# Kernel tuning notes

Hardware: AMD Instinct MI355X
Metric: run time of the kernel (lower is better)

Reference implementation:

```python
import jax, jax.numpy as jnp
import numpy as np

BIT = 128
Y_P = 0.5
RIGHT = BIT / 8.0
LEFT = RIGHT / 2.0
UB = BIT / 2.0
ALPHA = 0.1
PCT_NUM, PCT_DEN = 9, 10  # percent = 9/10
C_COEF = (1.0 / RIGHT) * np.log(Y_P / (99.0 * (1.0 - Y_P)))  # slope c (constant since y_p fixed)
A_COEF = -1.0 / (LEFT * C_COEF) * np.log(99.0 * Y_P / (1.0 - Y_P))  # hard-branch factor a
# with y_p=0.5: d = -c*BP, g = -a*c*BP, so f_easy = c*(x-BP), f_hard = a*c*(x-BP)


def setup_inputs() -> dict:
    key = jax.random.key(0)
    k1, k2 = jax.random.split(key)
    N, C = 6144, 200
    u = jax.random.normal(k1, (N, BIT), dtype=jnp.float32)
    labels = jax.random.randint(k2, (N,), 0, C)
    y = jax.nn.one_hot(labels, C, dtype=jnp.int32)
    ind = jnp.arange(N, dtype=jnp.int32)  # unused dataset indices
    return {"u": u, "y": y, "ind": ind}


def reference(u, y, ind):
    sg = jax.lax.stop_gradient
    N = u.shape[0]
    uh = jnp.tanh(u)
    s = (y @ y.T) > 0                      # [N,N] bool similarity (diagonal is True)
    inner = uh @ uh.T                      # [N,N]
    n_sim = s.sum(axis=1)                  # int per-row similar count
    n_dis = N - n_sim
    fn_sim = n_sim.astype(jnp.float32)
    fn_dis = n_dis.astype(jnp.float32)
    idx = jnp.arange(N)[None, :]

    meanS = jnp.clip(jnp.where(s, inner, 0.0).sum(1) / jnp.maximum(fn_sim, 1.0), 0.0, UB)
    meanDS = jnp.clip(jnp.where(s, 0.0, inner).sum(1) / jnp.maximum(fn_dis, 1.0), 0.0, UB)

    dis_sorted = jnp.sort(jnp.where(s, -jnp.inf, inner), axis=1)
    start_dis = (n_dis * PCT_NUM) // PCT_DEN          # int(len*0.9)
    tail_mask = idx >= (N - n_dis + start_dis)[:, None]
    tail_cnt = jnp.maximum((n_dis - start_dis).astype(jnp.float32), 1.0)
    dMax = jnp.clip(jnp.where(tail_mask, dis_sorted, 0.0).sum(1) / tail_cnt, 0.0, UB)

    sim_sorted = jnp.sort(jnp.where(s, inner, jnp.inf), axis=1)
    start_sim = (n_sim * PCT_NUM) // PCT_DEN
    head_mask = idx < (n_sim - start_sim)[:, None]
    head_cnt = jnp.maximum((n_sim - start_sim).astype(jnp.float32), 1.0)
    sMin = jnp.clip(jnp.where(head_mask, sim_sorted, 0.0).sum(1) / head_cnt, 0.0, UB)

    # .item() in the original detaches these -> stop_gradient
    meanS, meanDS, dMax, sMin = map(sg, (meanS, meanDS, dMax, sMin))
    BP = meanS - (UB - meanS) / UB * jnp.abs(meanS - dMax)      # [N]
    BPd = meanDS + meanDS / UB * jnp.abs(meanDS - sMin)         # [N]

    # similar-pair loss: f + log(1+exp(-f)) == softplus(f)
    dc = inner - BP[:, None]
    f_sim = jnp.where(inner > BP[:, None], C_COEF * dc, A_COEF * C_COEF * dc)
    mask_sim = s & (inner != BP[:, None])             # == BP excluded in torch indexing
    cnt_sim = jnp.maximum(mask_sim.sum(1).astype(jnp.float32), 1.0)
    row_pos = jnp.where(mask_sim, jax.nn.softplus(f_sim), 0.0).sum(1) / cnt_sim

    # dissimilar-pair loss: log(1+exp(-f)) == softplus(-f)
    dcd = inner - BPd[:, None]
    f_dis = jnp.where(inner < BPd[:, None], C_COEF * dcd, A_COEF * C_COEF * dcd)
    mask_dis = (~s) & (inner != BPd[:, None])
    cnt_dis = jnp.maximum(mask_dis.sum(1).astype(jnp.float32), 1.0)
    row_neg = jnp.where(mask_dis, jax.nn.softplus(-f_dis), 0.0).sum(1) / cnt_dis

    valid = (n_sim > 0) & (n_dis > 0)
    count = valid.sum().astype(jnp.float32)
    posL = jnp.where(count > 0, jnp.where(valid, row_pos, 0.0).sum() / jnp.maximum(count, 1.0), 0.0)
    navL = jnp.where(count > 0, jnp.where(valid, row_neg, 0.0).sum() / jnp.maximum(count, 1.0), 0.0)

    q_loss = ALPHA * jnp.mean((uh - jnp.sign(uh)) ** 2)
    return posL + navL + q_loss
```

## Files before the change

kernel.cpp:

```cpp
#include <hip/hip_runtime.h>
#include <cstdint>

#define NROW 6144
#define KDIM 128
#define NLAB 200
#define C_COEF (-0.28719499063341177f)
#define UBV 64.0f

typedef _Float16 f16x8 __attribute__((ext_vector_type(8)));
typedef float f32x4 __attribute__((ext_vector_type(4)));
typedef __attribute__((address_space(1))) const void as1c_void;
typedef __attribute__((address_space(3))) void as3_void;

__device__ __forceinline__ float softplus_f(float x){
  return fmaxf(x, 0.f) + __logf(1.f + __expf(-fabsf(x)));
}
__device__ __forceinline__ float waveRedF(float v){
#pragma unroll
  for (int o = 32; o; o >>= 1) v += __shfl_down(v, o, 64);
  return v;
}
__device__ __forceinline__ float bfRedF(float v){
#pragma unroll
  for (int o = 32; o; o >>= 1) v += __shfl_xor(v, o, 64);
  return v;
}
__device__ __forceinline__ int bfRedI(int v){
#pragma unroll
  for (int o = 32; o; o >>= 1) v += __shfl_xor(v, o, 64);
  return v;
}
__device__ __forceinline__ int bfMaxI(int v){
#pragma unroll
  for (int o = 32; o; o >>= 1){ int x = __shfl_xor(v, o, 64); v = v > x ? v : x; }
  return v;
}
__device__ __forceinline__ float bfMaxF(float v){
#pragma unroll
  for (int o = 32; o; o >>= 1) v = fmaxf(v, __shfl_xor(v, o, 64));
  return v;
}
__device__ __forceinline__ int bucket_of(float v){
  int b = (int)floorf(v * 2.f) + 128;
  return b < 0 ? 0 : (b > 255 ? 255 : b);
}

__global__ void k_label(const int* __restrict__ y, unsigned char* __restrict__ lab,
                        int* __restrict__ cnt){
  const int row = blockIdx.x;
  const int t = threadIdx.x;
  if (t < NLAB){
    if (y[(size_t)row * NLAB + t] != 0){
      lab[row] = (unsigned char)t;
      atomicAdd(&cnt[t], 1);
    }
  }
}

__global__ __launch_bounds__(192) void k_clsmask(const unsigned char* __restrict__ lab,
                                                 unsigned* __restrict__ cm){
  const int c = blockIdx.x;
  const int w = threadIdx.x;
  const uint4* p = (const uint4*)(lab + w * 32);
  uint4 a = p[0], b = p[1];
  unsigned words[8] = {a.x, a.y, a.z, a.w, b.x, b.y, b.z, b.w};
  unsigned bits = 0;
#pragma unroll
  for (int j = 0; j < 8; j++)
#pragma unroll
    for (int i = 0; i < 4; i++)
      if (((words[j] >> (8 * i)) & 255u) == (unsigned)c) bits |= 1u << (4 * j + i);
  cm[c * 192 + w] = bits;
}

__global__ __launch_bounds__(256) void k_tanh(const float* __restrict__ u,
    _Float16* __restrict__ uhswz, float* __restrict__ accf){
  const int tid = threadIdx.x;
  const int gid = blockIdx.x * 256 + tid;
  const int row = gid >> 4;
  const int h = gid & 15;
  const int g = h ^ (row & 7);
  const float* sp = u + (size_t)row * KDIM + g * 8;
  float q = 0.f;
  f16x8 o;
#pragma unroll
  for (int t = 0; t < 8; t++){
    float x = sp[t];
    float e2 = __expf(2.f * x);
    float th = 1.f - 2.f * __builtin_amdgcn_rcpf(e2 + 1.f);
    float sg = (th > 0.f) ? 1.f : ((th < 0.f) ? -1.f : 0.f);
    float d = th - sg;
    q += d * d;
    o[t] = (_Float16)th;
  }
  *(f16x8*)(uhswz + (size_t)row * KDIM + h * 8) = o;
  q = waveRedF(q);
  __shared__ float qb[4];
  if ((tid & 63) == 0) qb[tid >> 6] = q;
  __syncthreads();
  if (tid == 0) atomicAdd(&accf[0], qb[0] + qb[1] + qb[2] + qb[3]);
}

__global__ __launch_bounds__(256) void k_mm(const _Float16* __restrict__ A,
    _Float16* __restrict__ out, int row0){
  __shared__ __align__(16) _Float16 SH[2 * 128 * KDIM];
  _Float16* As = SH;
  _Float16* Bs = SH + 128 * KDIM;
  const int tid = threadIdx.x;
  const int wav = tid >> 6, lane = tid & 63;
  const int bj = blockIdx.x, bi = blockIdx.y;

  const char* Ag = (const char*)(A + (size_t)(row0 + bi * 128) * KDIM);
  const char* Bg = (const char*)(A + (size_t)(bj * 128) * KDIM);
  char* Asb = (char*)As;
  char* Bsb = (char*)Bs;
#pragma unroll
  for (int t = 0; t < 8; t++){
    const int ub = wav * 8192 + t * 1024;
    __builtin_amdgcn_global_load_lds((as1c_void*)(Ag + ub + lane * 16),
                                     (as3_void*)(Asb + ub), 16, 0, 0);
    __builtin_amdgcn_global_load_lds((as1c_void*)(Bg + ub + lane * 16),
                                     (as3_void*)(Bsb + ub), 16, 0, 0);
  }
  __syncthreads();

  const int quad = lane >> 4, l16 = lane & 15;
  const int wm = (wav >> 1) * 64, wn = (wav & 1) * 64;
  f32x4 acc[4][4];
#pragma unroll
  for (int im = 0; im < 4; im++)
#pragma unroll
    for (int in = 0; in < 4; in++)
      acc[im][in] = (f32x4){0.f, 0.f, 0.f, 0.f};

#pragma unroll
  for (int kb = 0; kb < 4; kb++){
    f16x8 af[4], bf[4];
#pragma unroll
    for (int i = 0; i < 4; i++){
      const int m = wm + i * 16 + l16;
      const int gidx = kb * 4 + quad;
      af[i] = *(const f16x8*)(Asb + m * 256 + ((gidx ^ (m & 7)) << 4));
      const int n = wn + i * 16 + l16;
      bf[i] = *(const f16x8*)(Bsb + n * 256 + ((gidx ^ (n & 7)) << 4));
    }
#pragma unroll
    for (int im = 0; im < 4; im++)
#pragma unroll
      for (int in = 0; in < 4; in++)
        acc[im][in] = __builtin_amdgcn_mfma_f32_16x16x32_f16(af[im], bf[in], acc[im][in], 0, 0, 0);
  }
  __syncthreads();

  _Float16* Cs = SH;
#pragma unroll
  for (int im = 0; im < 4; im++)
#pragma unroll
    for (int in = 0; in < 4; in++)
#pragma unroll
      for (int r = 0; r < 4; r++){
        const int rl = wm + im * 16 + quad * 4 + r;
        const int cl = wn + in * 16 + l16;
        Cs[rl * 132 + cl] = (_Float16)acc[im][in][r];
      }
  __syncthreads();

  _Float16* obase = out + (size_t)(bi * 128) * NROW + (size_t)bj * 128;
  const int s = tid & 15;
#pragma unroll
  for (int i = 0; i < 8; i++){
    const int r = (tid >> 4) + i * 16;
    f16x8 vv = *(const f16x8*)(Cs + r * 132 + s * 8);
    *(f16x8*)(obase + (size_t)r * NROW + s * 8) = vv;
  }
}

__global__ __launch_bounds__(256) void k_stats(const _Float16* __restrict__ buf,
    const unsigned char* __restrict__ lab, const int* __restrict__ cnt,
    const unsigned* __restrict__ cm,
    float* __restrict__ rowRes, int row0){
  __shared__ int   histS[4][256];
  __shared__ float simvS[4][512];
  __shared__ float candS[4][512];
  const int tid = threadIdx.x;
  const int lane = tid & 63;
  const int wav = tid >> 6;
  const int lrow = blockIdx.x * 4 + wav;
  const int row = row0 + lrow;
  const int myl = lab[row];
  const int n_sim = cnt[myl];
  const int n_dis = NROW - n_sim;
  if (n_dis == 0 || n_sim == 0) return;
  const int k1 = n_dis - (n_dis * 9) / 10;
  const int k2 = n_sim - (n_sim * 9) / 10;

  int*   hist = histS[wav];
  float* simv = simvS[wav];
  float* cand = candS[wav];
  *(int4*)&hist[lane * 4] = make_int4(0, 0, 0, 0);

  const f16x8* src = (const f16x8*)(buf + (size_t)lrow * NROW);
  const unsigned char* mrow = (const unsigned char*)(cm + (size_t)myl * 192);
  const unsigned long long below = (1ull << lane) - 1ull;

  float sumS = 0.f, sumD = 0.f;
  int nsB = 0;
#pragma unroll 1
  for (int it = 0; it < 12; ++it){
    f16x8 h8 = src[it * 64 + lane];
    unsigned m8 = (unsigned)mrow[it * 64 + lane];
#pragma unroll
    for (int e = 0; e < 8; e++){
      float v = (float)h8[e];
      bool sim = (m8 >> e) & 1u;
      unsigned long long bm = __ballot(sim);
      int pos = nsB + __builtin_popcountll(bm & below);
      nsB += __builtin_popcountll(bm);
      if (sim){
        sumS += v;
        if (pos < 512) simv[pos] = v;
      } else {
        sumD += v;
        atomicAdd(&hist[bucket_of(v)], 1);
      }
    }
  }
  sumS = bfRedF(sumS);
  sumD = bfRedF(sumD);
  const int ns = nsB < 512 ? nsB : 512;

  int cArr[4];
  cArr[0] = hist[4 * lane];
  cArr[1] = hist[4 * lane + 1];
  cArr[2] = hist[4 * lane + 2];
  cArr[3] = hist[4 * lane + 3];
  int part = cArr[0] + cArr[1] + cArr[2] + cArr[3];
  int suf = part;
#pragma unroll
  for (int o = 1; o < 64; o <<= 1){
    int x = __shfl_down(suf, o, 64);
    if (lane + o < 64) suf += x;
  }
  int cum = suf - part;
  int enc = -1, krF = 0;
#pragma unroll
  for (int d = 3; d >= 0; --d){
    int cd = cArr[d];
    if (k1 > cum && k1 <= cum + cd){
      enc = ((4 * lane + d) << 16) | cd;
      krF = k1 - cum;
    }
    cum += cd;
  }
  enc = bfMaxI(enc);
  const int kr0 = bfMaxI(krF);
  const int pb = enc >> 16;
  const int cntB = enc & 0xffff;
  const float thrLo = (pb == 0)   ? -1e30f : (float)(pb - 128) * 0.5f;
  const float thrHi = (pb == 255) ?  1e30f : (float)(pb - 127) * 0.5f;
  const bool small = (cntB <= 512);

  float sAb = 0.f;
  int ncB = 0;
#pragma unroll 1
  for (int it = 0; it < 12; ++it){
    f16x8 h8 = src[it * 64 + lane];
    unsigned m8 = (unsigned)mrow[it * 64 + lane];
#pragma unroll
    for (int e = 0; e < 8; e++){
      float v = (float)h8[e];
      bool dis = !((m8 >> e) & 1u);
      if (dis && v >= thrHi) sAb += v;
      bool inB = small && dis && v >= thrLo && v < thrHi;
      unsigned long long bm = __ballot(inB);
      int pos = ncB + __builtin_popcountll(bm & below);
      ncB += __builtin_popcountll(bm);
      if (inB) cand[pos] = v;
    }
  }
  sAb = bfRedF(sAb);

  float dSum;
  if (small){
    const int nc = ncB;
    float fpiv = -3e38f; int fgt = 0;
    for (int t = lane; t < nc; t += 64){
      float vt = cand[t];
      int gt = 0, eq = 0;
      for (int j = 0; j < nc; j++){
        float vj = cand[j];
        gt += (vj > vt); eq += (vj == vt);
      }
      if (gt < kr0 && kr0 <= gt + eq){ fpiv = vt; fgt = gt; }
    }
    const float piv = bfMaxF(fpiv);
    const int gtS = bfMaxI(fgt);
    float sg = 0.f;
    for (int t = lane; t < nc; t += 64){
      float v = cand[t];
      if (v > piv) sg += v;
    }
    sg = bfRedF(sg);
    dSum = sAb + sg + (float)(kr0 - gtS) * piv;
  } else {
    float lo = fmaxf(thrLo, -129.f), hi = fminf(thrHi, 129.f);
#pragma unroll 1
    for (int itr = 0; itr < 30; ++itr){
      float mid = 0.5f * (lo + hi);
      int cgt = 0;
#pragma unroll 1
      for (int it = 0; it < 12; ++it){
        f16x8 h8 = src[it * 64 + lane];
        unsigned m8 = (unsigned)mrow[it * 64 + lane];
#pragma unroll
        for (int e = 0; e < 8; e++){
          float v = (float)h8[e];
          bool dis = !((m8 >> e) & 1u);
          if (dis && v >= thrLo && v < thrHi && v > mid) cgt++;
        }
      }
      cgt = bfRedI(cgt);
      if (cgt >= kr0) lo = mid; else hi = mid;
    }
    const float piv = lo;
    float sg = 0.f; int cg = 0;
#pragma unroll 1
    for (int it = 0; it < 12; ++it){
      f16x8 h8 = src[it * 64 + lane];
      unsigned m8 = (unsigned)mrow[it * 64 + lane];
#pragma unroll
      for (int e = 0; e < 8; e++){
        float v = (float)h8[e];
        bool dis = !((m8 >> e) & 1u);
        if (dis && v >= thrLo && v < thrHi && v > piv){ sg += v; cg++; }
      }
    }
    sg = bfRedF(sg); cg = bfRedI(cg);
    dSum = sAb + sg + (float)(kr0 - cg) * piv;
  }

  float fpiv2 = -3e38f; int flt = 0;
  for (int t = lane; t < ns; t += 64){
    float vt = simv[t];
    int lt = 0, eq = 0;
    for (int j = 0; j < ns; j++){
      float vj = simv[j];
      lt += (vj < vt); eq += (vj == vt);
    }
    if (lt < k2 && k2 <= lt + eq){ fpiv2 = vt; flt = lt; }
  }
  const float piv2 = bfMaxF(fpiv2);
  const int ltS = bfMaxI(flt);
  float slt = 0.f;
  for (int t = lane; t < ns; t += 64){
    float v = simv[t];
    if (v < piv2) slt += v;
  }
  slt = bfRedF(slt);
  const float sSum = slt + (float)(k2 - ltS) * piv2;

  const float meanS  = fminf(fmaxf(sumS / fmaxf((float)n_sim, 1.f), 0.f), UBV);
  const float meanDS = fminf(fmaxf(sumD / fmaxf((float)n_dis, 1.f), 0.f), UBV);
  const float dMax   = fminf(fmaxf(dSum / fmaxf((float)k1, 1.f), 0.f), UBV);
  const float sMin   = fminf(fmaxf(sSum / fmaxf((float)k2, 1.f), 0.f), UBV);
  const float BP  = meanS - (UBV - meanS) / UBV * fabsf(meanS - dMax);
  const float BPd = meanDS + meanDS / UBV * fabsf(meanDS - sMin);

  float an = 0.f, cn = 0.f;
#pragma unroll 1
  for (int it = 0; it < 12; ++it){
    f16x8 h8 = src[it * 64 + lane];
    unsigned m8 = (unsigned)mrow[it * 64 + lane];
#pragma unroll
    for (int e = 0; e < 8; e++){
      float v = (float)h8[e];
      float dcd = v - BPd;
      float f = (v < BPd) ? C_COEF * dcd : (2.f * C_COEF) * dcd;
      float sp = softplus_f(-f);
      bool use = !((m8 >> e) & 1u) && (v != BPd);
      an += use ? sp : 0.f;
      cn += use ? 1.f : 0.f;
    }
  }
  float ap = 0.f, cp = 0.f;
  for (int t = lane; t < ns; t += 64){
    float v = simv[t];
    if (v != BP){
      float dc = v - BP;
      float f = (v > BP) ? C_COEF * dc : (2.f * C_COEF) * dc;
      ap += softplus_f(f); cp += 1.f;
    }
  }
  ap = bfRedF(ap); an = bfRedF(an);
  cp = bfRedF(cp); cn = bfRedF(cn);
  if (lane == 0){
    float4 r;
    r.x = ap / fmaxf(cp, 1.f);
    r.y = an / fmaxf(cn, 1.f);
    r.z = 1.f;
    r.w = 0.f;
    *(float4*)(rowRes + 4 * (size_t)row) = r;
  }
}

__global__ __launch_bounds__(256) void k_final(const float* __restrict__ accf,
    const float* __restrict__ rowRes, float* __restrict__ out){
  const int tid = threadIdx.x;
  float p = 0.f, n = 0.f, c = 0.f;
  for (int i = tid; i < NROW; i += 256){
    float4 r = *(const float4*)(rowRes + 4 * (size_t)i);
    p += r.x; n += r.y; c += r.z;
  }
  p = bfRedF(p); n = bfRedF(n); c = bfRedF(c);
  __shared__ float sb[12];
  const int wav = tid >> 6;
  if ((tid & 63) == 0){ sb[wav] = p; sb[4 + wav] = n; sb[8 + wav] = c; }
  __syncthreads();
  if (tid == 0){
    p = sb[0] + sb[1] + sb[2] + sb[3];
    n = sb[4] + sb[5] + sb[6] + sb[7];
    c = sb[8] + sb[9] + sb[10] + sb[11];
    float posL = 0.f, navL = 0.f;
    if (c > 0.f){ posL = p / c; navL = n / c; }
    out[0] = posL + navL + 0.1f * (accf[0] / (float)(NROW * KDIM));
  }
}

extern "C" void kernel_launch(void* const* d_in, const int* in_sizes, int n_in,
                              void* d_out, int out_size, void* d_ws, size_t ws_size,
                              hipStream_t stream){
  const float* u = (const float*)d_in[0];
  const int* y = (const int*)d_in[1];
  char* ws = (char*)d_ws;
  float* accf = (float*)ws;
  int* cnt = (int*)(ws + 64);
  unsigned char* lab = (unsigned char*)(ws + 4096);
  unsigned* cmask = (unsigned*)(ws + 12288);
  float* rowRes = (float*)(ws + 165888);
  _Float16* uhswz = (_Float16*)(ws + 264192);
  const size_t ibufOff = 264192 + (size_t)NROW * KDIM * 2;
  _Float16* ibuf = (_Float16*)(ws + ibufOff);

  hipMemsetAsync(d_ws, 0, 264192, stream);
  k_label<<<NROW, 256, 0, stream>>>(y, lab, cnt);
  k_clsmask<<<NLAB, 192, 0, stream>>>(lab, cmask);
  k_tanh<<<(NROW * 16) / 256, 256, 0, stream>>>(u, uhswz, accf);

  size_t avail = (ws_size > ibufOff) ? ws_size - ibufOff : 0;
  long maxRows = (long)(avail / ((size_t)NROW * 2));
  maxRows = (maxRows / 128) * 128;
  if (maxRows > NROW) maxRows = NROW;
  if (maxRows < 128) maxRows = 128;

  for (int r0 = 0; r0 < NROW; r0 += (int)maxRows){
    int rows = NROW - r0;
    if (rows > maxRows) rows = (int)maxRows;
    k_mm<<<dim3(48, rows / 128), 256, 0, stream>>>(uhswz, ibuf, r0);
    k_stats<<<rows / 4, 256, 0, stream>>>(ibuf, lab, cnt, cmask, rowRes, r0);
  }
  k_final<<<1, 256, 0, stream>>>(accf, rowRes, (float*)d_out);
}
```

Before: 199.7 us.

## Replace dissimilar top-k selection with two-level fp16 radix histogram

The top-10% dissimilar selection now runs as a two-pass radix select on the fp16 bit patterns. The first pass histograms the high byte over all entries and subtracts the similar entries, which are gathered through a per-class index list built in k_label. The second pass histograms the low byte inside the pivot bucket, giving an exact pivot with no O(n^2) candidate ranking and no 30-iteration bisection fallback. This removes the per-element ballots and mask reads, at the cost of two LDS atomics per element and a larger workspace memset.

After: 178.8 us. 1.12x faster.

```diff
diff --git a/kernel.cpp b/kernel.cpp
--- a/kernel.cpp
+++ b/kernel.cpp
@@ -12,6 +12,9 @@
 typedef __attribute__((address_space(1))) const void as1c_void;
 typedef __attribute__((address_space(3))) void as3_void;
 
+union U8 { f16x8 h; unsigned u[4]; };
+union CV16 { _Float16 h; unsigned short us; };
+
 __device__ __forceinline__ float softplus_f(float x){
   return fmaxf(x, 0.f) + __logf(1.f + __expf(-fabsf(x)));
 }
@@ -25,11 +28,6 @@
   for (int o = 32; o; o >>= 1) v += __shfl_xor(v, o, 64);
   return v;
 }
-__device__ __forceinline__ int bfRedI(int v){
-#pragma unroll
-  for (int o = 32; o; o >>= 1) v += __shfl_xor(v, o, 64);
-  return v;
-}
 __device__ __forceinline__ int bfMaxI(int v){
 #pragma unroll
   for (int o = 32; o; o >>= 1){ int x = __shfl_xor(v, o, 64); v = v > x ? v : x; }
@@ -40,19 +38,21 @@
   for (int o = 32; o; o >>= 1) v = fmaxf(v, __shfl_xor(v, o, 64));
   return v;
 }
-__device__ __forceinline__ int bucket_of(float v){
-  int b = (int)floorf(v * 2.f) + 128;
-  return b < 0 ? 0 : (b > 255 ? 255 : b);
+__device__ __forceinline__ float val_of_key(unsigned key){
+  unsigned bits = (key & 0x8000u) ? (key ^ 0x8000u) : (key ^ 0xFFFFu);
+  CV16 cv; cv.us = (unsigned short)bits;
+  return (float)cv.h;
 }
 
 __global__ void k_label(const int* __restrict__ y, unsigned char* __restrict__ lab,
-                        int* __restrict__ cnt){
+                        int* __restrict__ cnt, int* __restrict__ simIdx){
   const int row = blockIdx.x;
   const int t = threadIdx.x;
   if (t < NLAB){
     if (y[(size_t)row * NLAB + t] != 0){
       lab[row] = (unsigned char)t;
-      atomicAdd(&cnt[t], 1);
+      int p = atomicAdd(&cnt[t], 1);
+      if (p < 512) simIdx[t * 512 + p] = row;
     }
   }
 }
@@ -177,11 +177,10 @@
 
 __global__ __launch_bounds__(256) void k_stats(const _Float16* __restrict__ buf,
     const unsigned char* __restrict__ lab, const int* __restrict__ cnt,
-    const unsigned* __restrict__ cm,
+    const int* __restrict__ simIdx, const unsigned* __restrict__ cm,
     float* __restrict__ rowRes, int row0){
   __shared__ int   histS[4][256];
   __shared__ float simvS[4][512];
-  __shared__ float candS[4][512];
   const int tid = threadIdx.x;
   const int lane = tid & 63;
   const int wav = tid >> 6;
@@ -193,47 +192,55 @@
   if (n_dis == 0 || n_sim == 0) return;
   const int k1 = n_dis - (n_dis * 9) / 10;
   const int k2 = n_sim - (n_sim * 9) / 10;
+  const int ns = (n_sim < 512) ? n_sim : 512;
 
   int*   hist = histS[wav];
   float* simv = simvS[wav];
-  float* cand = candS[wav];
   *(int4*)&hist[lane * 4] = make_int4(0, 0, 0, 0);
 
   const f16x8* src = (const f16x8*)(buf + (size_t)lrow * NROW);
+  const _Float16* srcs = buf + (size_t)lrow * NROW;
   const unsigned char* mrow = (const unsigned char*)(cm + (size_t)myl * 192);
-  const unsigned long long below = (1ull << lane) - 1ull;
-
-  float sumS = 0.f, sumD = 0.f;
-  int nsB = 0;
+
+  float sumAll = 0.f;
 #pragma unroll 1
   for (int it = 0; it < 12; ++it){
-    f16x8 h8 = src[it * 64 + lane];
-    unsigned m8 = (unsigned)mrow[it * 64 + lane];
-#pragma unroll
-    for (int e = 0; e < 8; e++){
-      float v = (float)h8[e];
-      bool sim = (m8 >> e) & 1u;
-      unsigned long long bm = __ballot(sim);
-      int pos = nsB + __builtin_popcountll(bm & below);
-      nsB += __builtin_popcountll(bm);
-      if (sim){
-        sumS += v;
-        if (pos < 512) simv[pos] = v;
-      } else {
-        sumD += v;
-        atomicAdd(&hist[bucket_of(v)], 1);
-      }
-    }
-  }
+    U8 x; x.h = src[it * 64 + lane];
+#pragma unroll
+    for (int k = 0; k < 4; k++){
+      unsigned wv = x.u[k];
+      unsigned m = (wv >> 15) & 0x00010001u;
+      unsigned key2 = wv ^ 0x80008000u ^ (m * 0x7FFFu);
+      atomicAdd(&hist[(key2 >> 8) & 0xFFu], 1);
+      atomicAdd(&hist[key2 >> 24], 1);
+      sumAll += (float)x.h[2 * k] + (float)x.h[2 * k + 1];
+    }
+  }
+
+  float sumS = 0.f;
+  unsigned skey[8]; float sval[8];
+#pragma unroll
+  for (int j = 0; j < 8; j++){
+    const int t = lane + 64 * j;
+    skey[j] = 0xFFFFFFFFu; sval[j] = 0.f;
+    if (t < ns){
+      int idx = simIdx[myl * 512 + t];
+      CV16 cv; cv.h = srcs[idx];
+      unsigned bits = cv.us;
+      unsigned key = bits ^ 0x8000u ^ ((bits >> 15) * 0x7FFFu);
+      float v = (float)cv.h;
+      simv[t] = v; sumS += v;
+      atomicAdd(&hist[key >> 8], -1);
+      skey[j] = key; sval[j] = v;
+    }
+  }
+  sumAll = bfRedF(sumAll);
   sumS = bfRedF(sumS);
-  sumD = bfRedF(sumD);
-  const int ns = nsB < 512 ? nsB : 512;
+  const float sumD = sumAll - sumS;
 
   int cArr[4];
-  cArr[0] = hist[4 * lane];
-  cArr[1] = hist[4 * lane + 1];
-  cArr[2] = hist[4 * lane + 2];
-  cArr[3] = hist[4 * lane + 3];
+  { int4 c4 = *(const int4*)&hist[lane * 4];
+    cArr[0] = c4.x; cArr[1] = c4.y; cArr[2] = c4.z; cArr[3] = c4.w; }
   int part = cArr[0] + cArr[1] + cArr[2] + cArr[3];
   int suf = part;
 #pragma unroll
@@ -242,102 +249,74 @@
     if (lane + o < 64) suf += x;
   }
   int cum = suf - part;
-  int enc = -1, krF = 0;
+  int encB = -1, krF = 0;
 #pragma unroll
   for (int d = 3; d >= 0; --d){
     int cd = cArr[d];
-    if (k1 > cum && k1 <= cum + cd){
-      enc = ((4 * lane + d) << 16) | cd;
-      krF = k1 - cum;
-    }
+    if (k1 > cum && k1 <= cum + cd){ encB = 4 * lane + d; krF = k1 - cum; }
     cum += cd;
   }
-  enc = bfMaxI(enc);
-  const int kr0 = bfMaxI(krF);
-  const int pb = enc >> 16;
-  const int cntB = enc & 0xffff;
-  const float thrLo = (pb == 0)   ? -1e30f : (float)(pb - 128) * 0.5f;
-  const float thrHi = (pb == 255) ?  1e30f : (float)(pb - 127) * 0.5f;
-  const bool small = (cntB <= 512);
+  const int hbStar = bfMaxI(encB);
+  const int kr1 = bfMaxI(krF);
+
+  *(int4*)&hist[lane * 4] = make_int4(0, 0, 0, 0);
 
   float sAb = 0.f;
-  int ncB = 0;
 #pragma unroll 1
   for (int it = 0; it < 12; ++it){
-    f16x8 h8 = src[it * 64 + lane];
-    unsigned m8 = (unsigned)mrow[it * 64 + lane];
-#pragma unroll
-    for (int e = 0; e < 8; e++){
-      float v = (float)h8[e];
-      bool dis = !((m8 >> e) & 1u);
-      if (dis && v >= thrHi) sAb += v;
-      bool inB = small && dis && v >= thrLo && v < thrHi;
-      unsigned long long bm = __ballot(inB);
-      int pos = ncB + __builtin_popcountll(bm & below);
-      ncB += __builtin_popcountll(bm);
-      if (inB) cand[pos] = v;
+    U8 x; x.h = src[it * 64 + lane];
+#pragma unroll
+    for (int k = 0; k < 4; k++){
+      unsigned wv = x.u[k];
+      unsigned m = (wv >> 15) & 0x00010001u;
+      unsigned key2 = wv ^ 0x80008000u ^ (m * 0x7FFFu);
+      int hbLo = (key2 >> 8) & 0xFF;
+      int hbHi = key2 >> 24;
+      if (hbLo > hbStar) sAb += (float)x.h[2 * k];
+      else if (hbLo == hbStar) atomicAdd(&hist[key2 & 0xFFu], 1);
+      if (hbHi > hbStar) sAb += (float)x.h[2 * k + 1];
+      else if (hbHi == hbStar) atomicAdd(&hist[(key2 >> 16) & 0xFFu], 1);
+    }
+  }
+#pragma unroll
+  for (int j = 0; j < 8; j++){
+    if (skey[j] != 0xFFFFFFFFu){
+      int hb = (int)(skey[j] >> 8);
+      if (hb > hbStar) sAb -= sval[j];
+      else if (hb == hbStar) atomicAdd(&hist[skey[j] & 0xFFu], -1);
     }
   }
   sAb = bfRedF(sAb);
 
-  float dSum;
-  if (small){
-    const int nc = ncB;
-    float fpiv = -3e38f; int fgt = 0;
-    for (int t = lane; t < nc; t += 64){
-      float vt = cand[t];
-      int gt = 0, eq = 0;
-      for (int j = 0; j < nc; j++){
-        float vj = cand[j];
-        gt += (vj > vt); eq += (vj == vt);
-      }
-      if (gt < kr0 && kr0 <= gt + eq){ fpiv = vt; fgt = gt; }
-    }
-    const float piv = bfMaxF(fpiv);
-    const int gtS = bfMaxI(fgt);
-    float sg = 0.f;
-    for (int t = lane; t < nc; t += 64){
-      float v = cand[t];
-      if (v > piv) sg += v;
-    }
-    sg = bfRedF(sg);
-    dSum = sAb + sg + (float)(kr0 - gtS) * piv;
-  } else {
-    float lo = fmaxf(thrLo, -129.f), hi = fminf(thrHi, 129.f);
-#pragma unroll 1
-    for (int itr = 0; itr < 30; ++itr){
-      float mid = 0.5f * (lo + hi);
-      int cgt = 0;
-#pragma unroll 1
-      for (int it = 0; it < 12; ++it){
-        f16x8 h8 = src[it * 64 + lane];
-        unsigned m8 = (unsigned)mrow[it * 64 + lane];
-#pragma unroll
-        for (int e = 0; e < 8; e++){
-          float v = (float)h8[e];
-          bool dis = !((m8 >> e) & 1u);
-          if (dis && v >= thrLo && v < thrHi && v > mid) cgt++;
-        }
-      }
-      cgt = bfRedI(cgt);
-      if (cgt >= kr0) lo = mid; else hi = mid;
-    }
-    const float piv = lo;
-    float sg = 0.f; int cg = 0;
-#pragma unroll 1
-    for (int it = 0; it < 12; ++it){
-      f16x8 h8 = src[it * 64 + lane];
-      unsigned m8 = (unsigned)mrow[it * 64 + lane];
-#pragma unroll
-      for (int e = 0; e < 8; e++){
-        float v = (float)h8[e];
-        bool dis = !((m8 >> e) & 1u);
-        if (dis && v >= thrLo && v < thrHi && v > piv){ sg += v; cg++; }
-      }
-    }
-    sg = bfRedF(sg); cg = bfRedI(cg);
-    dSum = sAb + sg + (float)(kr0 - cg) * piv;
-  }
+  int c2[4];
+  { int4 c4 = *(const int4*)&hist[lane * 4];
+    c2[0] = c4.x; c2[1] = c4.y; c2[2] = c4.z; c2[3] = c4.w; }
+  part = c2[0] + c2[1] + c2[2] + c2[3];
+  suf = part;
+#pragma unroll
+  for (int o = 1; o < 64; o <<= 1){
+    int x = __shfl_down(suf, o, 64);
+    if (lane + o < 64) suf += x;
+  }
+  cum = suf - part;
+  int encL = -1, g2F = 0;
+#pragma unroll
+  for (int d = 3; d >= 0; --d){
+    int cd = c2[d];
+    if (kr1 > cum && kr1 <= cum + cd){ encL = 4 * lane + d; g2F = cum; }
+    cum += cd;
+  }
+  const int lbStar = bfMaxI(encL);
+  const int gt2 = bfMaxI(g2F);
+  float sumIn = 0.f;
+#pragma unroll
+  for (int d = 0; d < 4; d++){
+    int lb = 4 * lane + d;
+    if (lb > lbStar) sumIn += (float)c2[d] * val_of_key((unsigned)((hbStar << 8) | lb));
+  }
+  sumIn = bfRedF(sumIn);
+  const float piv = val_of_key((unsigned)((hbStar << 8) | lbStar));
+  const float dSum = sAb + sumIn + (float)(kr1 - gt2) * piv;
 
   float fpiv2 = -3e38f; int flt = 0;
   for (int t = lane; t < ns; t += 64){
@@ -435,14 +414,15 @@
   float* accf = (float*)ws;
   int* cnt = (int*)(ws + 64);
   unsigned char* lab = (unsigned char*)(ws + 4096);
-  unsigned* cmask = (unsigned*)(ws + 12288);
-  float* rowRes = (float*)(ws + 165888);
-  _Float16* uhswz = (_Float16*)(ws + 264192);
-  const size_t ibufOff = 264192 + (size_t)NROW * KDIM * 2;
+  int* simIdx = (int*)(ws + 12288);
+  unsigned* cmask = (unsigned*)(ws + 421888);
+  float* rowRes = (float*)(ws + 575488);
+  _Float16* uhswz = (_Float16*)(ws + 673792);
+  const size_t ibufOff = 673792 + (size_t)NROW * KDIM * 2;
   _Float16* ibuf = (_Float16*)(ws + ibufOff);
 
-  hipMemsetAsync(d_ws, 0, 264192, stream);
-  k_label<<<NROW, 256, 0, stream>>>(y, lab, cnt);
+  hipMemsetAsync(d_ws, 0, 673792, stream);
+  k_label<<<NROW, 256, 0, stream>>>(y, lab, cnt, simIdx);
   k_clsmask<<<NLAB, 192, 0, stream>>>(lab, cmask);
   k_tanh<<<(NROW * 16) / 256, 256, 0, stream>>>(u, uhswz, accf);
 
@@ -456,7 +436,7 @@
     int rows = NROW - r0;
     if (rows > maxRows) rows = (int)maxRows;
     k_mm<<<dim3(48, rows / 128), 256, 0, stream>>>(uhswz, ibuf, r0);
-    k_stats<<<rows / 4, 256, 0, stream>>>(ibuf, lab, cnt, cmask, rowRes, r0);
+    k_stats<<<rows / 4, 256, 0, stream>>>(ibuf, lab, cnt, simIdx, cmask, rowRes, r0);
   }
   k_final<<<1, 256, 0, stream>>>(accf, rowRes, (float*)d_out);
 }
```
